# Kernel tuning notes

Measured on AMD Instinct MI355X. Metric: run time of the kernel, lower is better.

Reference implementation:

```python
import jax, jax.numpy as jnp
import numpy as np

WS = 8          # window size (square)
N_TOK = WS * WS # tokens per window
DIM = 256
HEADS = 8
HEAD_DIM = DIM // HEADS
B_WIN = 4096    # batch * num_windows


def _rel_pos_index(ws):
    # Same construction as the torch code (meshgrid 'ij').
    coords = np.stack(np.meshgrid(np.arange(ws), np.arange(ws), indexing='ij'))  # [2,ws,ws]
    flat = coords.reshape(2, -1)                        # [2, ws*ws]
    rel = flat[:, :, None] - flat[:, None, :]           # [2, N, N]
    rel = rel.transpose(1, 2, 0).astype(np.int64)       # [N, N, 2]
    rel[..., 0] += ws - 1
    rel[..., 1] += ws - 1
    rel[..., 0] *= 2 * ws - 1
    return rel.sum(-1)                                  # [N, N]

REL_IDX = jnp.asarray(_rel_pos_index(WS))               # [64, 64] int


def setup_inputs() -> dict:
    key = jax.random.key(0)
    ks = jax.random.split(key, 9)
    inner = DIM
    std = 0.02
    x = jax.random.normal(ks[0], (B_WIN, N_TOK, DIM), dtype=jnp.float32)
    # Linear weights stored as [in, out] for x @ W
    wq = jax.random.normal(ks[1], (DIM, inner), dtype=jnp.float32) * std
    bq = jnp.zeros((inner,), dtype=jnp.float32)
    wkv = jax.random.normal(ks[2], (DIM, 2 * inner), dtype=jnp.float32) * std
    bkv = jnp.zeros((2 * inner,), dtype=jnp.float32)
    table = jax.random.normal(ks[3], ((2 * WS - 1) * (2 * WS - 1), HEADS), dtype=jnp.float32) * std
    wp = jax.random.normal(ks[4], (DIM, DIM), dtype=jnp.float32) * std
    bp = jnp.zeros((DIM,), dtype=jnp.float32)
    return {"x": x, "wq": wq, "bq": bq, "wkv": wkv, "bkv": bkv,
            "table": table, "wp": wp, "bp": bp}


def reference(x, wq, bq, wkv, bkv, table, wp, bp):
    B, N, C = x.shape
    H, hd = HEADS, HEAD_DIM
    scale = hd ** -0.5
    # q/k/v projections: [B, N, C] -> [B, H, N, hd]
    q = (x @ wq + bq).reshape(B, N, H, hd).transpose(0, 2, 1, 3)
    kv = (x @ wkv + bkv).reshape(B, N, 2, H, hd).transpose(2, 0, 3, 1, 4)
    k, v = kv[0], kv[1]
    attn = jnp.einsum('bhnd,bhmd->bhnm', q * scale, k)  # [B, H, N, N]
    # relative position bias gather: [N, N, H] -> [H, N, N]
    bias = table[REL_IDX].transpose(2, 0, 1)
    attn = jax.nn.softmax(attn + bias[None], axis=-1)
    out = jnp.einsum('bhnm,bhmd->bhnd', attn, v)        # [B, H, N, hd]
    out = out.transpose(0, 2, 1, 3).reshape(B, N, C)
    return out @ wp + bp
```

## Files before the change

kernel.cpp:

```cpp
#include <hip/hip_runtime.h>

typedef unsigned short u16;
typedef __attribute__((ext_vector_type(8))) __bf16 bf16x8;
typedef __attribute__((ext_vector_type(4))) float f32x4;

#define SCALE 0.17677669529663687f

#define ATTN_OFF   0ull
#define WSTORE_OFF 134217728ull
#define WPT_OFF    134610944ull
#define TABF_OFF   134742016ull

__device__ __forceinline__ u16 f2bf(float f) {
  __bf16 h = (__bf16)f;
  return __builtin_bit_cast(u16, h);
}

__device__ __forceinline__ void gload16(const void* g, void* l) {
  __builtin_amdgcn_global_load_lds(
      (const __attribute__((address_space(1))) unsigned int*)g,
      (__attribute__((address_space(3))) unsigned int*)l, 16, 0, 0);
}

__device__ __forceinline__ f32x4 mfma16(bf16x8 a, bf16x8 b, f32x4 c) {
  return __builtin_amdgcn_mfma_f32_16x16x32_bf16(a, b, c, 0, 0, 0);
}

__global__ __launch_bounds__(256) void prep_kernel(
    const float* __restrict__ wq, const float* __restrict__ wkv,
    const float* __restrict__ wp, const float* __restrict__ table,
    u16* __restrict__ Wstore, u16* __restrict__ wpT, float* __restrict__ tabf)
{
  int i = blockIdx.x * 256 + threadIdx.x;
  if (i < 196608) {
    int h = i / 24576, r = i % 24576;
    int ks = r / 6144, r2 = r % 6144;
    int col = r2 / 64, wi = r2 % 64;
    int kl = ((wi * 2) ^ ((col & 7) << 4)) >> 1;
    int k = ks * 64 + kl;
    int n = (col < 32) ? h * 32 + col
          : (col < 64) ? 256 + h * 32 + (col - 32)
                       : 512 + h * 32 + (col - 64);
    float v = (n < 256) ? wq[k * 256 + n] : wkv[k * 512 + (n - 256)];
    if (col < 32) v *= SCALE;
    Wstore[i] = f2bf(v);
  } else if (i < 262144) {
    int j = i - 196608;
    int n = j >> 8, k = j & 255;
    wpT[n * 256 + k] = f2bf(wp[k * 256 + n]);
  } else if (i < 263944) {
    int j = i - 262144;
    int h = j / 225, r = j % 225;
    tabf[h * 256 + r] = table[r * 8 + h];
  }
}

__global__ __launch_bounds__(256, 2) void kf_kernel(
    const float* __restrict__ x, const u16* __restrict__ Wstore,
    const float* __restrict__ bq, const float* __restrict__ bkv,
    const float* __restrict__ tabf, u16* __restrict__ attnout)
{
  __shared__ char smem[50176];
  char* Wt  = smem;
  char* Pb  = smem + 12288;
  char* Qb2 = smem + 24576;
  char* Kb2 = smem + 32768;
  char* Vb2 = smem + 40960;
  char* Tb  = smem + 49152;

  const int tid  = threadIdx.x;
  const int lane = tid & 63;
  const int w    = tid >> 6;
  const int c    = lane & 15;
  const int s4   = lane >> 4;
  const int wwin = w >> 1;
  const int rbase = (w & 1) * 32;
  const int b    = blockIdx.x;
  const f32x4 fzero = {0.f, 0.f, 0.f, 0.f};

  bf16x8 xf[2][8];
  {
    const float* xw = x + ((size_t)b * 2 + wwin) * 16384;
#pragma unroll
    for (int rt = 0; rt < 2; ++rt) {
      int t = rbase + rt * 16 + c;
#pragma unroll
      for (int kc = 0; kc < 8; ++kc) {
        const float* p = xw + t * 256 + kc * 32 + s4 * 8;
        float4 v0 = *(const float4*)p;
        float4 v1 = *(const float4*)(p + 4);
        bf16x8 f;
        f[0] = (__bf16)v0.x; f[1] = (__bf16)v0.y;
        f[2] = (__bf16)v0.z; f[3] = (__bf16)v0.w;
        f[4] = (__bf16)v1.x; f[5] = (__bf16)v1.y;
        f[6] = (__bf16)v1.z; f[7] = (__bf16)v1.w;
        xf[rt][kc] = f;
      }
    }
  }

  const char* wsrc = (const char*)Wstore;
#define STAGE(t, bufi)                                                    \
  {                                                                       \
    const char* _s = wsrc + (size_t)(t) * 12288 + w * 1024 + lane * 16;   \
    char* _d = Wt + (bufi) * 12288 + w * 1024;                            \
    gload16(_s, _d);                                                      \
    gload16(_s + 4096, _d + 4096);                                        \
    gload16(_s + 8192, _d + 8192);                                        \
  }

  STAGE(0, 0);
  __syncthreads();

#pragma unroll 1
  for (int h = 0; h < 8; ++h) {
    *(float*)(Tb + tid * 4) = tabf[h * 256 + tid];

    f32x4 acc[2][6];
#pragma unroll
    for (int rt = 0; rt < 2; ++rt)
#pragma unroll
      for (int nc = 0; nc < 6; ++nc) acc[rt][nc] = fzero;

#pragma unroll
    for (int ks = 0; ks < 4; ++ks) {
      const int t = h * 4 + ks;
      if (t + 1 < 32) STAGE(t + 1, (t + 1) & 1);
      const char* bb = Wt + (t & 1) * 12288;
#pragma unroll
      for (int kk = 0; kk < 2; ++kk) {
        bf16x8 bfr[6];
#pragma unroll
        for (int nc = 0; nc < 6; ++nc) {
          int col = nc * 16 + c;
          bfr[nc] = *(const bf16x8*)(bb + col * 128 +
                                     ((kk * 64 + s4 * 16) ^ ((c & 7) << 4)));
        }
#pragma unroll
        for (int rt = 0; rt < 2; ++rt)
#pragma unroll
          for (int nc = 0; nc < 6; ++nc)
            acc[rt][nc] = mfma16(xf[rt][ks * 2 + kk], bfr[nc], acc[rt][nc]);
      }
      __syncthreads();
    }

    char* Qb = Qb2 + wwin * 4096;
    char* Kb = Kb2 + wwin * 4096;
    char* Vb = Vb2 + wwin * 4096;
#pragma unroll
    for (int nc = 0; nc < 6; ++nc) {
      int col = nc * 16 + c;
      float bias = (col < 32) ? bq[h * 32 + col] * SCALE
                 : (col < 64) ? bkv[h * 32 + (col - 32)]
                              : bkv[256 + h * 32 + (col - 64)];
#pragma unroll
      for (int rt = 0; rt < 2; ++rt)
#pragma unroll
        for (int q = 0; q < 4; ++q) {
          int t = rbase + rt * 16 + s4 * 4 + q;
          u16 val = f2bf(acc[rt][nc][q] + bias);
          if (col < 32)
            *(u16*)(Qb + t * 64 + ((col * 2) ^ (q << 4))) = val;
          else if (col < 64)
            *(u16*)(Kb + t * 64 + (((col - 32) * 2) ^ (q << 4))) = val;
          else {
            int d = col - 64;
            *(u16*)(Vb + d * 128 + ((t * 2) ^ ((c & 7) << 4))) = val;
          }
        }
    }
    __syncthreads();

    const char* Qh = Qb2 + wwin * 4096;
    const char* Kh = Kb2 + wwin * 4096;
    const char* Vh = Vb2 + wwin * 4096;
    char* Pw = Pb + w * 2048;

    bf16x8 aq[2];
#pragma unroll
    for (int rt = 0; rt < 2; ++rt) {
      int t = rbase + rt * 16 + c;
      aq[rt] = *(const bf16x8*)(Qh + t * 64 + ((s4 * 16) ^ ((c & 3) << 4)));
    }
    f32x4 sa[2][4];
#pragma unroll
    for (int nt = 0; nt < 4; ++nt) {
      int tk = nt * 16 + c;
      bf16x8 bk = *(const bf16x8*)(Kh + tk * 64 + ((s4 * 16) ^ ((c & 3) << 4)));
#pragma unroll
      for (int rt = 0; rt < 2; ++rt)
        sa[rt][nt] = mfma16(aq[rt], bk, fzero);
    }

#pragma unroll
    for (int rt = 0; rt < 2; ++rt)
#pragma unroll
      for (int q = 0; q < 4; ++q) {
        int n = rbase + rt * 16 + s4 * 4 + q;
#pragma unroll
        for (int nt = 0; nt < 4; ++nt) {
          int m = nt * 16 + c;
          int dr = (n >> 3) - (m >> 3) + 7;
          int dc = (n & 7) - (m & 7) + 7;
          sa[rt][nt][q] += *(const float*)(Tb + (dr * 15 + dc) * 4);
        }
      }

    float inv[2][4];
#pragma unroll
    for (int rt = 0; rt < 2; ++rt)
#pragma unroll
      for (int q = 0; q < 4; ++q) {
        float s0 = 0.f;
#pragma unroll
        for (int nt = 0; nt < 4; ++nt) {
          float pv = __expf(sa[rt][nt][q]);
          sa[rt][nt][q] = pv;
          s0 += pv;
        }
        s0 += __shfl_xor(s0, 1);
        s0 += __shfl_xor(s0, 2);
        s0 += __shfl_xor(s0, 4);
        s0 += __shfl_xor(s0, 8);
        inv[rt][q] = __builtin_amdgcn_rcpf(s0);
      }

    f32x4 oa[2][2];
#pragma unroll
    for (int rt = 0; rt < 2; ++rt) { oa[rt][0] = fzero; oa[rt][1] = fzero; }
#pragma unroll
    for (int half = 0; half < 2; ++half) {
#pragma unroll
      for (int rt = 0; rt < 2; ++rt)
#pragma unroll
        for (int q = 0; q < 4; ++q) {
          int lt = rt * 16 + s4 * 4 + q;
#pragma unroll
          for (int j = 0; j < 2; ++j) {
            int nt = half * 2 + j;
            int mcol = j * 16 + c;
            *(u16*)(Pw + lt * 64 + ((mcol * 2) ^ (q << 4))) =
                f2bf(sa[rt][nt][q] * inv[rt][q]);
          }
        }
      asm volatile("s_waitcnt lgkmcnt(0)" ::: "memory");
      __builtin_amdgcn_sched_barrier(0);
      bf16x8 ap[2];
#pragma unroll
      for (int rt = 0; rt < 2; ++rt) {
        int lt = rt * 16 + c;
        ap[rt] = *(const bf16x8*)(Pw + lt * 64 + ((s4 * 16) ^ ((c & 3) << 4)));
      }
#pragma unroll
      for (int d2 = 0; d2 < 2; ++d2) {
        int d = d2 * 16 + c;
        bf16x8 bv = *(const bf16x8*)(Vh + d * 128 +
                                     ((half * 64 + s4 * 16) ^ ((c & 7) << 4)));
#pragma unroll
        for (int rt = 0; rt < 2; ++rt)
          oa[rt][d2] = mfma16(ap[rt], bv, oa[rt][d2]);
      }
      if (half == 0) {
        asm volatile("s_waitcnt lgkmcnt(0)" ::: "memory");
        __builtin_amdgcn_sched_barrier(0);
      }
    }

    u16* ow = attnout + ((size_t)b * 2 + wwin) * 16384 + h * 32;
#pragma unroll
    for (int rt = 0; rt < 2; ++rt)
#pragma unroll
      for (int d2 = 0; d2 < 2; ++d2)
#pragma unroll
        for (int q = 0; q < 4; ++q) {
          int t = rbase + rt * 16 + s4 * 4 + q;
          ow[t * 256 + d2 * 16 + c] = f2bf(oa[rt][d2][q]);
        }

    __syncthreads();
  }
#undef STAGE
}

__global__ __launch_bounds__(256) void proj_kernel(
    const u16* __restrict__ A, const u16* __restrict__ wpT,
    const float* __restrict__ bp, float* __restrict__ out)
{
  __shared__ char smem[32768];
  char* As = smem;
  char* Bs = smem + 16384;
  const int tid = threadIdx.x, lane = tid & 63, w = tid >> 6;
  const int c = lane & 15, s4 = lane >> 4;
  const int m0 = (int)(blockIdx.x >> 1) * 128;
  const int n0 = (int)(blockIdx.x & 1) * 128;
  const int wr = w >> 1, wc = w & 1;
  const f32x4 fzero = {0.f, 0.f, 0.f, 0.f};

  f32x4 acc[4][4];
#pragma unroll
  for (int mt = 0; mt < 4; ++mt)
#pragma unroll
    for (int nt = 0; nt < 4; ++nt) acc[mt][nt] = fzero;

  for (int ks = 0; ks < 4; ++ks) {
    __syncthreads();
#pragma unroll
    for (int i = 0; i < 4; ++i) {
      int o = (w * 4 + i) * 1024 + lane * 16;
      int r = o >> 7, kb = o & 127;
      gload16((const char*)A + ((size_t)(m0 + r) * 256 + ks * 64) * 2 + kb,
              As + (w * 4 + i) * 1024);
      gload16((const char*)wpT + ((size_t)(n0 + r) * 256 + ks * 64) * 2 + kb,
              Bs + (w * 4 + i) * 1024);
    }
    __syncthreads();
#pragma unroll
    for (int kk = 0; kk < 2; ++kk) {
      bf16x8 af[4], bfr[4];
#pragma unroll
      for (int t4 = 0; t4 < 4; ++t4) {
        af[t4]  = *(const bf16x8*)(As + (wr * 64 + t4 * 16 + c) * 128 + kk * 64 + s4 * 16);
        bfr[t4] = *(const bf16x8*)(Bs + (wc * 64 + t4 * 16 + c) * 128 + kk * 64 + s4 * 16);
      }
#pragma unroll
      for (int mt = 0; mt < 4; ++mt)
#pragma unroll
        for (int nt = 0; nt < 4; ++nt)
          acc[mt][nt] = mfma16(af[mt], bfr[nt], acc[mt][nt]);
    }
  }

#pragma unroll
  for (int nt = 0; nt < 4; ++nt) {
    int col = n0 + wc * 64 + nt * 16 + c;
    float bpv = bp[col];
#pragma unroll
    for (int mt = 0; mt < 4; ++mt)
#pragma unroll
      for (int q = 0; q < 4; ++q) {
        int row = m0 + wr * 64 + mt * 16 + s4 * 4 + q;
        out[(size_t)row * 256 + col] = acc[mt][nt][q] + bpv;
      }
  }
}

extern "C" void kernel_launch(void* const* d_in, const int* in_sizes, int n_in,
                              void* d_out, int out_size, void* d_ws, size_t ws_size,
                              hipStream_t stream)
{
  const float* x     = (const float*)d_in[0];
  const float* wq    = (const float*)d_in[1];
  const float* bq    = (const float*)d_in[2];
  const float* wkv   = (const float*)d_in[3];
  const float* bkv   = (const float*)d_in[4];
  const float* table = (const float*)d_in[5];
  const float* wp    = (const float*)d_in[6];
  const float* bp    = (const float*)d_in[7];
  float* out = (float*)d_out;
  char* ws = (char*)d_ws;

  u16*   attnout = (u16*)(ws + ATTN_OFF);
  u16*   Wstore  = (u16*)(ws + WSTORE_OFF);
  u16*   wpT     = (u16*)(ws + WPT_OFF);
  float* tabf    = (float*)(ws + TABF_OFF);

  prep_kernel<<<1032, 256, 0, stream>>>(wq, wkv, wp, table, Wstore, wpT, tabf);
  kf_kernel<<<2048, 256, 0, stream>>>(x, Wstore, bq, bkv, tabf, attnout);
  proj_kernel<<<4096, 256, 0, stream>>>(attnout, wpT, bp, out);
}
```

Baseline: 344.3 us.

## Fuse output projection into attention kernel and simplify table prep indexing

Removes the separate projection kernel. Each attention block now runs the output-projection GEMM on its own 128 rows after its attention loop: it reloads the bf16 attention output it just wrote, which should still be in cache, multiplies by the transposed projection weights in two 128-column halves, and writes the final fp32 output. This saves one kernel launch and the extra pass over the intermediate. The cost is more registers and a longer attention kernel, which could hurt occupancy, and it depends on the block seeing its own global writes after a barrier. The prep kernel's table-transpose indexing also switches from div/mod to shifts, with a slightly larger grid.

```diff
diff --git a/kernel.cpp b/kernel.cpp
--- a/kernel.cpp
+++ b/kernel.cpp
@@ -48,17 +48,19 @@
     int j = i - 196608;
     int n = j >> 8, k = j & 255;
     wpT[n * 256 + k] = f2bf(wp[k * 256 + n]);
-  } else if (i < 263944) {
+  } else if (i < 264192) {
     int j = i - 262144;
-    int h = j / 225, r = j % 225;
-    tabf[h * 256 + r] = table[r * 8 + h];
+    int h = j >> 8, r = j & 255;
+    if (r < 225) tabf[h * 256 + r] = table[r * 8 + h];
   }
 }
 
 __global__ __launch_bounds__(256, 2) void kf_kernel(
     const float* __restrict__ x, const u16* __restrict__ Wstore,
     const float* __restrict__ bq, const float* __restrict__ bkv,
-    const float* __restrict__ tabf, u16* __restrict__ attnout)
+    const float* __restrict__ tabf, u16* __restrict__ attnout,
+    const u16* __restrict__ wpT, const float* __restrict__ bp,
+    float* __restrict__ out)
 {
   __shared__ char smem[50176];
   char* Wt  = smem;
@@ -281,67 +283,66 @@
     __syncthreads();
   }
 #undef STAGE
-}
-
-__global__ __launch_bounds__(256) void proj_kernel(
-    const u16* __restrict__ A, const u16* __restrict__ wpT,
-    const float* __restrict__ bp, float* __restrict__ out)
-{
-  __shared__ char smem[32768];
-  char* As = smem;
-  char* Bs = smem + 16384;
-  const int tid = threadIdx.x, lane = tid & 63, w = tid >> 6;
-  const int c = lane & 15, s4 = lane >> 4;
-  const int m0 = (int)(blockIdx.x >> 1) * 128;
-  const int n0 = (int)(blockIdx.x & 1) * 128;
-  const int wr = w >> 1, wc = w & 1;
-  const f32x4 fzero = {0.f, 0.f, 0.f, 0.f};
-
-  f32x4 acc[4][4];
-#pragma unroll
-  for (int mt = 0; mt < 4; ++mt)
-#pragma unroll
-    for (int nt = 0; nt < 4; ++nt) acc[mt][nt] = fzero;
-
-  for (int ks = 0; ks < 4; ++ks) {
-    __syncthreads();
-#pragma unroll
-    for (int i = 0; i < 4; ++i) {
-      int o = (w * 4 + i) * 1024 + lane * 16;
-      int r = o >> 7, kb = o & 127;
-      gload16((const char*)A + ((size_t)(m0 + r) * 256 + ks * 64) * 2 + kb,
-              As + (w * 4 + i) * 1024);
-      gload16((const char*)wpT + ((size_t)(n0 + r) * 256 + ks * 64) * 2 + kb,
-              Bs + (w * 4 + i) * 1024);
-    }
-    __syncthreads();
-#pragma unroll
-    for (int kk = 0; kk < 2; ++kk) {
-      bf16x8 af[4], bfr[4];
-#pragma unroll
-      for (int t4 = 0; t4 < 4; ++t4) {
-        af[t4]  = *(const bf16x8*)(As + (wr * 64 + t4 * 16 + c) * 128 + kk * 64 + s4 * 16);
-        bfr[t4] = *(const bf16x8*)(Bs + (wc * 64 + t4 * 16 + c) * 128 + kk * 64 + s4 * 16);
-      }
+
+  {
+    char* As = smem;
+    char* Bs = smem + 16384;
+    const int m0 = b * 128;
+    const int wr2 = w >> 1, wc2 = w & 1;
+#pragma unroll 1
+    for (int nh = 0; nh < 2; ++nh) {
+      const int n0 = nh * 128;
+      f32x4 pacc[4][4];
 #pragma unroll
       for (int mt = 0; mt < 4; ++mt)
 #pragma unroll
-        for (int nt = 0; nt < 4; ++nt)
-          acc[mt][nt] = mfma16(af[mt], bfr[nt], acc[mt][nt]);
-    }
-  }
-
-#pragma unroll
-  for (int nt = 0; nt < 4; ++nt) {
-    int col = n0 + wc * 64 + nt * 16 + c;
-    float bpv = bp[col];
-#pragma unroll
-    for (int mt = 0; mt < 4; ++mt)
-#pragma unroll
-      for (int q = 0; q < 4; ++q) {
-        int row = m0 + wr * 64 + mt * 16 + s4 * 4 + q;
-        out[(size_t)row * 256 + col] = acc[mt][nt][q] + bpv;
-      }
+        for (int nt = 0; nt < 4; ++nt) pacc[mt][nt] = fzero;
+
+      for (int ks = 0; ks < 4; ++ks) {
+        __syncthreads();
+#pragma unroll
+        for (int i = 0; i < 4; ++i) {
+          int o = (w * 4 + i) * 1024 + lane * 16;
+          int r = o >> 7, kb = o & 127;
+          gload16((const char*)attnout +
+                      ((size_t)(m0 + r) * 256 + ks * 64) * 2 + kb,
+                  As + (w * 4 + i) * 1024);
+          gload16((const char*)wpT +
+                      ((size_t)(n0 + r) * 256 + ks * 64) * 2 + kb,
+                  Bs + (w * 4 + i) * 1024);
+        }
+        __syncthreads();
+#pragma unroll
+        for (int kk = 0; kk < 2; ++kk) {
+          bf16x8 af[4], bf2[4];
+#pragma unroll
+          for (int t4 = 0; t4 < 4; ++t4) {
+            af[t4]  = *(const bf16x8*)(As + (wr2 * 64 + t4 * 16 + c) * 128 +
+                                       kk * 64 + s4 * 16);
+            bf2[t4] = *(const bf16x8*)(Bs + (wc2 * 64 + t4 * 16 + c) * 128 +
+                                       kk * 64 + s4 * 16);
+          }
+#pragma unroll
+          for (int mt = 0; mt < 4; ++mt)
+#pragma unroll
+            for (int nt = 0; nt < 4; ++nt)
+              pacc[mt][nt] = mfma16(af[mt], bf2[nt], pacc[mt][nt]);
+        }
+      }
+
+#pragma unroll
+      for (int nt = 0; nt < 4; ++nt) {
+        int col = n0 + wc2 * 64 + nt * 16 + c;
+        float bpv = bp[col];
+#pragma unroll
+        for (int mt = 0; mt < 4; ++mt)
+#pragma unroll
+          for (int q = 0; q < 4; ++q) {
+            int row = m0 + wr2 * 64 + mt * 16 + s4 * 4 + q;
+            out[(size_t)row * 256 + col] = pacc[mt][nt][q] + bpv;
+          }
+      }
+    }
   }
 }
 
@@ -365,7 +366,7 @@
   u16*   wpT     = (u16*)(ws + WPT_OFF);
   float* tabf    = (float*)(ws + TABF_OFF);
 
-  prep_kernel<<<1032, 256, 0, stream>>>(wq, wkv, wp, table, Wstore, wpT, tabf);
-  kf_kernel<<<2048, 256, 0, stream>>>(x, Wstore, bq, bkv, tabf, attnout);
-  proj_kernel<<<4096, 256, 0, stream>>>(attnout, wpT, bp, out);
-}
+  prep_kernel<<<1040, 256, 0, stream>>>(wq, wkv, wp, table, Wstore, wpT, tabf);
+  kf_kernel<<<2048, 256, 0, stream>>>(x, Wstore, bq, bkv, tabf, attnout,
+                                      wpT, bp, out);
+}
```

Result: faster. 308.6 us, median of 2 (-10.4%).
